# Kernel tuning notes

Measured on AMD Instinct MI355X. Metric: run time of the kernel, lower is better.

Reference implementation:

```python
import jax, jax.numpy as jnp
import numpy as np

N = 30000      # nodes
E = 480000     # edges (before self-loops)
D = 100        # hidden_dim / in_channels
H = 4          # heads
PH = 100       # per-head dim
L = 6          # layers
G = 128        # graphs in batch
NUM_ATOM = 100
OUT_DIM = 64


def _xavier(k, shape, gain=1.0):
    fan_in, fan_out = shape[-1], shape[-2]
    lim = gain * np.sqrt(6.0 / (fan_in + fan_out))
    return jax.random.uniform(k, shape, jnp.float32, -lim, lim)


def setup_inputs() -> dict:
    key = jax.random.key(0)
    ks = jax.random.split(key, 12)
    x = jax.random.randint(ks[0], (N,), 0, NUM_ATOM)
    edge_index = jax.random.randint(ks[1], (2, E), 0, N)
    edge_attr = jax.random.normal(ks[2], (E, D), dtype=jnp.float32)
    batch = jnp.sort(jax.random.randint(ks[3], (N,), 0, G))
    emb = _xavier(ks[4], (NUM_ATOM, D))
    W = _xavier(ks[5], (L, H * PH, D))
    We = _xavier(ks[6], (L, H * PH, D))
    a = _xavier(ks[7], (L, H, 2 * PH), gain=1.414)
    ln_g = jnp.ones((L, D), jnp.float32)
    ln_b = jnp.zeros((L, D), jnp.float32)
    w1 = _xavier(ks[8], (OUT_DIM, D))
    b1 = jnp.zeros((OUT_DIM,), jnp.float32)
    w2 = _xavier(ks[9], (1, OUT_DIM))
    b2 = jnp.zeros((1,), jnp.float32)
    return dict(x=x, edge_index=edge_index, edge_attr=edge_attr, batch=batch,
                emb=emb, W=W, We=We, a=a, ln_g=ln_g, ln_b=ln_b,
                w1=w1, b1=b1, w2=w2, b2=b2)


def _forward(x, edge_index, edge_attr, batch, emb, W, We, a, ln_g, ln_b, w1, b1, w2, b2):
    n = x.shape[0]
    loop = jnp.arange(n)
    src = jnp.concatenate([edge_index[0], loop])            # [E']
    dst = jnp.concatenate([edge_index[1], loop])            # [E']  (target, softmax key)
    ea = jnp.concatenate([edge_attr, jnp.zeros((n, D), edge_attr.dtype)], axis=0)  # self-loop attr = 0
    h = emb[x]                                              # [N, D]
    for l in range(L):
        hx = (h @ W[l].T).reshape(n, H, PH)                 # [N, H, PH]
        he = (ea @ We[l].T).reshape(-1, H, PH)              # [E', H, PH]
        a_i, a_j = a[l][:, :PH], a[l][:, PH:]               # [H, PH] each
        # alpha = sum(a * [x_i ; x_j + edge_attr]) split into two dots
        score_i = jnp.einsum('nhd,hd->nh', hx, a_i)         # [N, H]
        xj = hx[src]                                        # [E', H, PH]
        alpha = score_i[dst] + jnp.einsum('ehd,hd->eh', xj + he, a_j)  # [E', H]
        alpha = jnp.where(alpha > 0, alpha, 0.2 * alpha)    # leaky_relu(0.2)
        # segment softmax over edges grouped by target node (every node has a self-loop)
        amax = jax.ops.segment_max(alpha, dst, num_segments=n)
        alpha = jnp.exp(alpha - amax[dst])
        denom = jax.ops.segment_sum(alpha, dst, num_segments=n)
        alpha = alpha / (denom[dst] + 1e-16)
        msg = (xj * alpha[..., None]).sum(axis=1)           # [E', PH] (heads summed, per module)
        aggr = jax.ops.segment_sum(msg, dst, num_segments=n)  # [N, PH]
        # LayerNorm(D), eps=1e-5
        mu = aggr.mean(-1, keepdims=True)
        var = ((aggr - mu) ** 2).mean(-1, keepdims=True)
        y = (aggr - mu) / jnp.sqrt(var + 1e-5) * ln_g[l] + ln_b[l]
        y = jax.nn.elu(y)                                   # dropout = identity (eval)
        h = y + h
    # global mean pool over graphs
    s = jax.ops.segment_sum(h, batch, num_segments=G)
    cnt = jax.ops.segment_sum(jnp.ones((n, 1), h.dtype), batch, num_segments=G)
    pooled = s / jnp.maximum(cnt, 1.0)
    hh = pooled @ w1.T + b1                                 # [G, 64]
    out = hh @ w2.T + b2                                    # [G, 1]
    return out, hh


def reference(x, edge_index, edge_attr, batch, emb, W, We, a, ln_g, ln_b, w1, b1, w2, b2):
    return _forward(x, edge_index, edge_attr, batch, emb, W, We, a, ln_g, ln_b, w1, b1, w2, b2)
```

## Files before the change

kernel.cpp:

```cpp
#include <hip/hip_runtime.h>
#include <cstdint>
#include <cstddef>

#define N_NODES 30000
#define N_EDGES 480000
#define EP_EDGES (N_EDGES + N_NODES)
#define DIM 100
#define NH 4
#define NL 6
#define NG 128
#define KP 416

#define OFF_H       0u
#define OFF_AGG2    12000000u
#define OFF_POS     12000000u
#define OFF_DEG     13920000u
#define OFF_CURS    14040000u
#define OFF_POOL    12000000u
#define OFF_CNT     12051200u
#define OFF_SCI     60000000u
#define OFF_SCJ     60480000u
#define OFF_ESC     60960000u
#define OFF_CWIJ    85440000u
#define OFF_CWE     85459200u
#define OFF_WR      85469184u
#define OFF_INDPTR  86429184u
#define OFF_CSRS    86549248u
#define OFF_BSUM    88589248u

typedef _Float16 half8 __attribute__((ext_vector_type(8)));
typedef float f32x4 __attribute__((ext_vector_type(4)));

static __device__ __forceinline__ unsigned short f2h(float f) {
  return __builtin_bit_cast(unsigned short, (_Float16)f);
}
static __device__ __forceinline__ float h2f(unsigned short u) {
  return (float)__builtin_bit_cast(_Float16, u);
}

__global__ __launch_bounds__(256) void k_init(const int* __restrict__ x,
                                              const float* __restrict__ emb,
                                              float* __restrict__ h,
                                              int* __restrict__ deg, int* __restrict__ cursor) {
  int tid = blockIdx.x * 256 + threadIdx.x;
  if (tid < N_NODES * DIM) {
    int n = tid / DIM;
    int d = tid - n * DIM;
    h[tid] = emb[x[n] * DIM + d];
  }
  if (tid < N_NODES) { deg[tid] = 0; cursor[tid] = 0; }
}

__global__ __launch_bounds__(256) void k_fold(const float* __restrict__ W,
                                              const float* __restrict__ We,
                                              const float* __restrict__ a,
                                              float* __restrict__ cWij, float* __restrict__ cWe) {
  int tid = blockIdx.x * 256 + threadIdx.x;
  if (tid < NL * DIM * 8) {
    int l = tid / 800, r = tid % 800;
    int k = r >> 3, c = r & 7;
    int hh = c & 3, isJ = c >> 2;
    const float* wp = W + (size_t)(l * 400 + hh * 100) * 100 + k;
    const float* ap = a + (size_t)(l * 4 + hh) * 200 + isJ * 100;
    float s = 0.f;
    for (int d = 0; d < 100; ++d) s += wp[(size_t)d * 100] * ap[d];
    cWij[l * 800 + k * 8 + c] = s;
  } else if (tid < NL * DIM * 8 + DIM * 24) {
    int m = tid - NL * DIM * 8;
    int k = m / 24, c = m % 24;
    int l = c >> 2, hh = c & 3;
    const float* wp = We + (size_t)(l * 400 + hh * 100) * 100 + k;
    const float* ap = a + (size_t)(l * 4 + hh) * 200 + 100;
    float s = 0.f;
    for (int d = 0; d < 100; ++d) s += wp[(size_t)d * 100] * ap[d];
    cWe[c * 104 + k] = s;
  }
}

__global__ __launch_bounds__(256) void k_bfrag(const float* __restrict__ W,
                                               unsigned short* __restrict__ Bfrag) {
  int tid = blockIdx.x * 256 + threadIdx.x;
  if (tid >= NL * 7 * 13 * 64 * 8) return;
  int j = tid & 7;
  int lane = (tid >> 3) & 63;
  int rest = tid >> 9;
  int ks = rest % 13;
  int rest2 = rest / 13;
  int ct = rest2 % 7;
  int l = rest2 / 7;
  int k = ks * 32 + ((lane >> 4) << 3) + j;
  int n = ct * 16 + (lane & 15);
  float v = 0.f;
  if (k < 400 && n < 100) {
    int hh = k / 100, kk = k - hh * 100;
    v = W[(size_t)(l * 400 + hh * 100 + n) * 100 + kk];
  }
  Bfrag[tid] = f2h(v);
}

__global__ __launch_bounds__(256) void k_deg(const int* __restrict__ ei, int* __restrict__ deg) {
  int tid = blockIdx.x * 256 + threadIdx.x;
  if (tid >= EP_EDGES) return;
  int dstn = (tid < N_EDGES) ? ei[N_EDGES + tid] : (tid - N_EDGES);
  atomicAdd(&deg[dstn], 1);
}

__global__ __launch_bounds__(1024) void k_scan1(const int* __restrict__ deg,
                                                int* __restrict__ indptr, int* __restrict__ bsum) {
  __shared__ int s[1024];
  int t = threadIdx.x;
  int i = blockIdx.x * 1024 + t;
  int v = (i < N_NODES) ? deg[i] : 0;
  s[t] = v;
  __syncthreads();
  for (int off = 1; off < 1024; off <<= 1) {
    int tmp = (t >= off) ? s[t - off] : 0;
    __syncthreads();
    s[t] += tmp;
    __syncthreads();
  }
  if (i < N_NODES) indptr[i + 1] = s[t];
  if (t == 1023) bsum[blockIdx.x] = s[1023];
}
__global__ __launch_bounds__(64) void k_scan2(int* __restrict__ bsum) {
  int t = threadIdx.x;
  int v = (t < 30) ? bsum[t] : 0;
  int inc = v;
  for (int off = 1; off < 64; off <<= 1) {
    int up = __shfl_up(inc, off);
    if (t >= off) inc += up;
  }
  if (t < 30) bsum[t] = inc - v;
}
__global__ __launch_bounds__(1024) void k_scan3(int* __restrict__ indptr,
                                                const int* __restrict__ bsum) {
  int i = blockIdx.x * 1024 + threadIdx.x;
  if (i < N_NODES) indptr[i + 1] += bsum[blockIdx.x];
  if (i == 0) indptr[0] = 0;
}

__global__ __launch_bounds__(256) void k_scatter(const int* __restrict__ ei,
                                                 const int* __restrict__ indptr,
                                                 int* __restrict__ cursor,
                                                 int* __restrict__ csr_src,
                                                 int* __restrict__ pos,
                                                 unsigned short* __restrict__ esc) {
  int tid = blockIdx.x * 256 + threadIdx.x;
  if (tid >= EP_EDGES) return;
  int dstn = (tid < N_EDGES) ? ei[N_EDGES + tid] : (tid - N_EDGES);
  int srcn = (tid < N_EDGES) ? ei[tid] : (tid - N_EDGES);
  int p = indptr[dstn] + atomicAdd(&cursor[dstn], 1);
  csr_src[p] = srcn;
  if (tid < N_EDGES) {
    pos[tid] = p;
  } else {
#pragma unroll
    for (int l = 0; l < NL; ++l) {
      ushort4 z; z.x = 0; z.y = 0; z.z = 0; z.w = 0;
      *(ushort4*)(esc + ((size_t)l * EP_EDGES + p) * 4) = z;
    }
  }
}

__global__ __launch_bounds__(384) void k_escore(const float* __restrict__ ea,
                                                const float* __restrict__ cWe,
                                                const int* __restrict__ pos,
                                                unsigned short* __restrict__ esc) {
  __shared__ __align__(16) float s_ea[64 * 100];
  int t = threadIdx.x;
  const float4* g4 = (const float4*)(ea + (size_t)blockIdx.x * 6400);
  float4* l4 = (float4*)s_ea;
  for (int i = t; i < 1600; i += 384) l4[i] = g4[i];
  __syncthreads();

  int slot = t & 63;
  int lg = __builtin_amdgcn_readfirstlane(t >> 6);
  const float* r0 = s_ea + slot * 100;
  const float* wl = cWe + (lg * 4) * 104;
  float acc0[4] = {0.f, 0.f, 0.f, 0.f};
#pragma unroll
  for (int k4 = 0; k4 < 25; ++k4) {
    float4 x0 = *(const float4*)(r0 + k4 * 4);
#pragma unroll
    for (int hh = 0; hh < 4; ++hh) {
      float4 w = *(const float4*)(wl + hh * 104 + k4 * 4);
      acc0[hh] = fmaf(x0.w, w.w, fmaf(x0.z, w.z, fmaf(x0.y, w.y, fmaf(x0.x, w.x, acc0[hh]))));
    }
  }
  int e0 = blockIdx.x * 64 + slot;
  int p0 = pos[e0];
  ushort4 o0;
  o0.x = f2h(acc0[0]); o0.y = f2h(acc0[1]); o0.z = f2h(acc0[2]); o0.w = f2h(acc0[3]);
  *(ushort4*)(esc + ((size_t)lg * EP_EDGES + p0) * 4) = o0;
}

__global__ __launch_bounds__(256) void k_score(const float* __restrict__ h,
                                               const float* __restrict__ cw,
                                               float* __restrict__ sc_i, float* __restrict__ sc_j) {
  __shared__ __align__(16) float s[DIM * 8];
  for (int i = threadIdx.x; i < DIM * 8; i += 256) s[i] = cw[i];
  __syncthreads();
  int n = blockIdx.x * 256 + threadIdx.x;
  if (n >= N_NODES) return;
  float acc[8] = {0.f, 0.f, 0.f, 0.f, 0.f, 0.f, 0.f, 0.f};
  const float* hr = h + (size_t)n * DIM;
  for (int k4 = 0; k4 < 25; ++k4) {
    float4 v = *(const float4*)(hr + k4 * 4);
    float vv[4] = {v.x, v.y, v.z, v.w};
#pragma unroll
    for (int kk = 0; kk < 4; ++kk) {
      const float* sr = s + (k4 * 4 + kk) * 8;
#pragma unroll
      for (int c = 0; c < 8; ++c) acc[c] += vv[kk] * sr[c];
    }
  }
  *(float4*)(sc_i + (size_t)n * 4) = make_float4(acc[0], acc[1], acc[2], acc[3]);
  *(float4*)(sc_j + (size_t)n * 4) = make_float4(acc[4], acc[5], acc[6], acc[7]);
}

#define ALPHA_P(pp)                                                                  \
  int s_ = csr_src[pp];                                                              \
  float4 sj_ = *(const float4*)(sc_j + (size_t)s_ * 4);                              \
  ushort4 eb_ = *(const ushort4*)(esc_l + (size_t)(pp) * 4);                         \
  float a0 = si.x + sj_.x + h2f(eb_.x); a0 = a0 > 0.f ? a0 : 0.2f * a0;              \
  float a1 = si.y + sj_.y + h2f(eb_.y); a1 = a1 > 0.f ? a1 : 0.2f * a1;              \
  float a2 = si.z + sj_.z + h2f(eb_.z); a2 = a2 > 0.f ? a2 : 0.2f * a2;              \
  float a3 = si.w + sj_.w + h2f(eb_.w); a3 = a3 > 0.f ? a3 : 0.2f * a3;

__global__ __launch_bounds__(256) void k_aggr(const float* __restrict__ h,
                                              const float* __restrict__ sc_i,
                                              const float* __restrict__ sc_j,
                                              const unsigned short* __restrict__ esc_l,
                                              const int* __restrict__ indptr,
                                              const int* __restrict__ csr_src,
                                              unsigned short* __restrict__ agg2h) {
  __shared__ __align__(16) uint4 s_pack[4][64];
  int wave = threadIdx.x >> 6;
  int lane = threadIdx.x & 63;
  int n = blockIdx.x * 4 + wave;
  int start = indptr[n], end = indptr[n + 1];
  int deg = end - start;
  float4 si = *(const float4*)(sc_i + (size_t)n * 4);
  float A0 = 0.f, A1 = 0.f, A2 = 0.f, A3 = 0.f;
  float B0 = 0.f, B1 = 0.f, B2 = 0.f, B3 = 0.f;
  bool has2 = lane < (DIM - 64);

  if (deg <= 64) {
    int p = start + lane;
    bool act = p < end;
    int srcr = 0;
    float a0 = -1e30f, a1 = -1e30f, a2 = -1e30f, a3 = -1e30f;
    if (act) {
      int s2 = csr_src[p];
      float4 sj2 = *(const float4*)(sc_j + (size_t)s2 * 4);
      ushort4 eb2 = *(const ushort4*)(esc_l + (size_t)p * 4);
      a0 = si.x + sj2.x + h2f(eb2.x); a0 = a0 > 0.f ? a0 : 0.2f * a0;
      a1 = si.y + sj2.y + h2f(eb2.y); a1 = a1 > 0.f ? a1 : 0.2f * a1;
      a2 = si.z + sj2.z + h2f(eb2.z); a2 = a2 > 0.f ? a2 : 0.2f * a2;
      a3 = si.w + sj2.w + h2f(eb2.w); a3 = a3 > 0.f ? a3 : 0.2f * a3;
      srcr = s2;
    }
    float m0 = a0, m1 = a1, m2 = a2, m3 = a3;
    for (int off = 32; off; off >>= 1) {
      m0 = fmaxf(m0, __shfl_xor(m0, off));
      m1 = fmaxf(m1, __shfl_xor(m1, off));
      m2 = fmaxf(m2, __shfl_xor(m2, off));
      m3 = fmaxf(m3, __shfl_xor(m3, off));
    }
    float e0 = act ? __expf(a0 - m0) : 0.f;
    float e1 = act ? __expf(a1 - m1) : 0.f;
    float e2 = act ? __expf(a2 - m2) : 0.f;
    float e3 = act ? __expf(a3 - m3) : 0.f;
    float d0 = e0, d1 = e1, d2 = e2, d3 = e3;
    for (int off = 32; off; off >>= 1) {
      d0 += __shfl_xor(d0, off); d1 += __shfl_xor(d1, off);
      d2 += __shfl_xor(d2, off); d3 += __shfl_xor(d3, off);
    }
    float w0 = e0 * (1.f / (d0 + 1e-16f));
    float w1 = e1 * (1.f / (d1 + 1e-16f));
    float w2 = e2 * (1.f / (d2 + 1e-16f));
    float w3 = e3 * (1.f / (d3 + 1e-16f));
    uint4 pk;
    pk.x = (unsigned)srcr;
    pk.y = (unsigned)f2h(w0) | ((unsigned)f2h(w1) << 16);
    pk.z = (unsigned)f2h(w2) | ((unsigned)f2h(w3) << 16);
    pk.w = 0u;
    s_pack[wave][lane] = pk;
    for (int j = 0; j < deg; ++j) {
      uint4 pk2 = s_pack[wave][j];
      int sj2 = (int)pk2.x;
      float q0 = h2f((unsigned short)(pk2.y & 0xffffu));
      float q1 = h2f((unsigned short)(pk2.y >> 16));
      float q2 = h2f((unsigned short)(pk2.z & 0xffffu));
      float q3 = h2f((unsigned short)(pk2.z >> 16));
      const float* hr = h + (size_t)sj2 * DIM;
      float hv0 = hr[lane];
      float hv1 = has2 ? hr[64 + lane] : 0.f;
      A0 += q0 * hv0; A1 += q1 * hv0; A2 += q2 * hv0; A3 += q3 * hv0;
      B0 += q0 * hv1; B1 += q1 * hv1; B2 += q2 * hv1; B3 += q3 * hv1;
    }
  } else {
    float m0 = -1e30f, m1 = -1e30f, m2 = -1e30f, m3 = -1e30f;
    for (int p = start + lane; p < end; p += 64) {
      ALPHA_P(p)
      (void)s_;
      m0 = fmaxf(m0, a0); m1 = fmaxf(m1, a1); m2 = fmaxf(m2, a2); m3 = fmaxf(m3, a3);
    }
    for (int off = 32; off; off >>= 1) {
      m0 = fmaxf(m0, __shfl_xor(m0, off));
      m1 = fmaxf(m1, __shfl_xor(m1, off));
      m2 = fmaxf(m2, __shfl_xor(m2, off));
      m3 = fmaxf(m3, __shfl_xor(m3, off));
    }
    float d0 = 0.f, d1 = 0.f, d2 = 0.f, d3 = 0.f;
    for (int p = start + lane; p < end; p += 64) {
      ALPHA_P(p)
      (void)s_;
      d0 += __expf(a0 - m0); d1 += __expf(a1 - m1);
      d2 += __expf(a2 - m2); d3 += __expf(a3 - m3);
    }
    for (int off = 32; off; off >>= 1) {
      d0 += __shfl_xor(d0, off); d1 += __shfl_xor(d1, off);
      d2 += __shfl_xor(d2, off); d3 += __shfl_xor(d3, off);
    }
    float i0 = 1.f / (d0 + 1e-16f), i1 = 1.f / (d1 + 1e-16f);
    float i2 = 1.f / (d2 + 1e-16f), i3 = 1.f / (d3 + 1e-16f);
    for (int base = start; base < end; base += 64) {
      int cntv = min(64, end - base);
      int p = base + lane;
      float w0 = 0.f, w1 = 0.f, w2 = 0.f, w3 = 0.f;
      int srcr = 0;
      if (p < end) {
        ALPHA_P(p)
        w0 = __expf(a0 - m0) * i0; w1 = __expf(a1 - m1) * i1;
        w2 = __expf(a2 - m2) * i2; w3 = __expf(a3 - m3) * i3;
        srcr = s_;
      }
      for (int j = 0; j < cntv; ++j) {
        int sj2 = __shfl(srcr, j);
        float q0 = __shfl(w0, j), q1 = __shfl(w1, j);
        float q2 = __shfl(w2, j), q3 = __shfl(w3, j);
        const float* hr = h + (size_t)sj2 * DIM;
        float hv0 = hr[lane];
        float hv1 = has2 ? hr[64 + lane] : 0.f;
        A0 += q0 * hv0; A1 += q1 * hv0; A2 += q2 * hv0; A3 += q3 * hv0;
        B0 += q0 * hv1; B1 += q1 * hv1; B2 += q2 * hv1; B3 += q3 * hv1;
      }
    }
  }
  unsigned short* outp = agg2h + (size_t)n * KP;
  outp[lane] = f2h(A0); outp[100 + lane] = f2h(A1);
  outp[200 + lane] = f2h(A2); outp[300 + lane] = f2h(A3);
  if (has2) {
    outp[64 + lane] = f2h(B0); outp[164 + lane] = f2h(B1);
    outp[264 + lane] = f2h(B2); outp[364 + lane] = f2h(B3);
  }
  if (lane < KP - 400) outp[400 + lane] = 0;
}

__global__ __launch_bounds__(256) void k_gemm2(const _Float16* __restrict__ agg2h,
                                               const _Float16* __restrict__ Bfrag_l,
                                               const float* __restrict__ lg,
                                               const float* __restrict__ lb,
                                               float* __restrict__ h) {
  int t = threadIdx.x;
  int lane = t & 63;
  int w = t >> 6;
  int c = lane & 15;
  int quad = lane >> 4;
  int nb = blockIdx.x * 64 + w * 16;

  f32x4 acc[7];
#pragma unroll
  for (int ct = 0; ct < 7; ++ct) acc[ct] = (f32x4){0.f, 0.f, 0.f, 0.f};

  const _Float16* arow = agg2h + (size_t)(nb + c) * KP + quad * 8;
#pragma unroll
  for (int ks = 0; ks < 13; ++ks) {
    half8 a = *(const half8*)(arow + ks * 32);
    const _Float16* bp = Bfrag_l + (size_t)(ks * 64 + lane) * 8;
#pragma unroll
    for (int ct = 0; ct < 7; ++ct) {
      half8 b = *(const half8*)(bp + (size_t)ct * 13 * 64 * 8);
      acc[ct] = __builtin_amdgcn_mfma_f32_16x16x32_f16(a, b, acc[ct], 0, 0, 0);
    }
  }

  float gv[7], bv[7];
#pragma unroll
  for (int ct = 0; ct < 7; ++ct) {
    int col = ct * 16 + c;
    gv[ct] = (col < DIM) ? lg[col] : 0.f;
    bv[ct] = (col < DIM) ? lb[col] : 0.f;
  }
  bool c4 = c < 4;
#pragma unroll
  for (int r = 0; r < 4; ++r) {
    int n = nb + quad * 4 + r;
    float v[7];
#pragma unroll
    for (int ct = 0; ct < 7; ++ct) v[ct] = acc[ct][r];
    float s = v[0] + v[1] + v[2] + v[3] + v[4] + v[5] + (c4 ? v[6] : 0.f);
    s += __shfl_xor(s, 1); s += __shfl_xor(s, 2);
    s += __shfl_xor(s, 4); s += __shfl_xor(s, 8);
    float mu = s * 0.01f;
    float dv[7];
    float s2 = 0.f;
#pragma unroll
    for (int ct = 0; ct < 6; ++ct) { dv[ct] = v[ct] - mu; s2 += dv[ct] * dv[ct]; }
    dv[6] = c4 ? (v[6] - mu) : 0.f;
    s2 += dv[6] * dv[6];
    s2 += __shfl_xor(s2, 1); s2 += __shfl_xor(s2, 2);
    s2 += __shfl_xor(s2, 4); s2 += __shfl_xor(s2, 8);
    float rstd = rsqrtf(s2 * 0.01f + 1e-5f);
    if (n < N_NODES) {
      float* hp = h + (size_t)n * DIM;
#pragma unroll
      for (int ct = 0; ct < 7; ++ct) {
        int col = ct * 16 + c;
        if (ct < 6 || c4) {
          float y = dv[ct] * rstd * gv[ct] + bv[ct];
          y = y > 0.f ? y : (__expf(y) - 1.f);
          hp[col] += y;
        }
      }
    }
  }
}

__global__ __launch_bounds__(128) void k_pool(const float* __restrict__ h,
                                              const int* __restrict__ batch,
                                              float* __restrict__ pooled, float* __restrict__ cnt) {
  int d = threadIdx.x;
  int n0 = blockIdx.x * 64;
  int n1 = min(n0 + 64, N_NODES);
  if (n0 >= N_NODES) return;
  int curg = -1;
  float acc = 0.f, c = 0.f;
  for (int n = n0; n < n1; ++n) {
    int g = batch[n];
    if (g != curg) {
      if (curg >= 0) {
        if (d < 100) atomicAdd(&pooled[(size_t)curg * DIM + d], acc);
        if (d == 0) atomicAdd(&cnt[curg], c);
      }
      curg = g; acc = 0.f; c = 0.f;
    }
    if (d < 100) acc += h[(size_t)n * DIM + d];
    c += 1.f;
  }
  if (curg >= 0) {
    if (d < 100) atomicAdd(&pooled[(size_t)curg * DIM + d], acc);
    if (d == 0) atomicAdd(&cnt[curg], c);
  }
}

__global__ __launch_bounds__(64) void k_mlp(const float* __restrict__ pooled,
                                            const float* __restrict__ cnt,
                                            const float* __restrict__ w1, const float* __restrict__ b1,
                                            const float* __restrict__ w2, const float* __restrict__ b2,
                                            float* __restrict__ out) {
  int g = blockIdx.x;
  int j = threadIdx.x;
  float invc = 1.0f / fmaxf(cnt[g], 1.0f);
  const float* pr = pooled + (size_t)g * DIM;
  const float* wr = w1 + (size_t)j * DIM;
  float acc = 0.f;
  for (int k = 0; k < DIM; ++k) acc += pr[k] * wr[k];
  float hh = acc * invc + b1[j];
  out[NG + g * 64 + j] = hh;
  float v = hh * w2[j];
  for (int off = 32; off; off >>= 1) v += __shfl_xor(v, off);
  if (j == 0) out[g] = v + b2[0];
}

extern "C" void kernel_launch(void* const* d_in, const int* in_sizes, int n_in,
                              void* d_out, int out_size, void* d_ws, size_t ws_size,
                              hipStream_t stream) {
  (void)in_sizes; (void)n_in; (void)out_size; (void)ws_size;
  const int* x = (const int*)d_in[0];
  const int* ei = (const int*)d_in[1];
  const float* ea = (const float*)d_in[2];
  const int* batch = (const int*)d_in[3];
  const float* emb = (const float*)d_in[4];
  const float* W = (const float*)d_in[5];
  const float* We = (const float*)d_in[6];
  const float* a = (const float*)d_in[7];
  const float* ln_g = (const float*)d_in[8];
  const float* ln_b = (const float*)d_in[9];
  const float* w1 = (const float*)d_in[10];
  const float* b1 = (const float*)d_in[11];
  const float* w2 = (const float*)d_in[12];
  const float* b2 = (const float*)d_in[13];
  float* outp = (float*)d_out;

  char* ws = (char*)d_ws;
  float* h = (float*)(ws + OFF_H);
  unsigned short* agg2h = (unsigned short*)(ws + OFF_AGG2);
  int* pos = (int*)(ws + OFF_POS);
  int* deg = (int*)(ws + OFF_DEG);
  int* cursor = (int*)(ws + OFF_CURS);
  float* pooled = (float*)(ws + OFF_POOL);
  float* cnt = (float*)(ws + OFF_CNT);
  float* sc_i = (float*)(ws + OFF_SCI);
  float* sc_j = (float*)(ws + OFF_SCJ);
  unsigned short* esc = (unsigned short*)(ws + OFF_ESC);
  float* cWij = (float*)(ws + OFF_CWIJ);
  float* cWe = (float*)(ws + OFF_CWE);
  unsigned short* Bfrag = (unsigned short*)(ws + OFF_WR);
  int* indptr = (int*)(ws + OFF_INDPTR);
  int* csr_src = (int*)(ws + OFF_CSRS);
  int* bsum = (int*)(ws + OFF_BSUM);

  k_init<<<11719, 256, 0, stream>>>(x, emb, h, deg, cursor);
  k_fold<<<29, 256, 0, stream>>>(W, We, a, cWij, cWe);
  k_bfrag<<<1092, 256, 0, stream>>>(W, Bfrag);
  k_deg<<<1993, 256, 0, stream>>>(ei, deg);
  k_scan1<<<30, 1024, 0, stream>>>(deg, indptr, bsum);
  k_scan2<<<1, 64, 0, stream>>>(bsum);
  k_scan3<<<30, 1024, 0, stream>>>(indptr, bsum);
  k_scatter<<<1993, 256, 0, stream>>>(ei, indptr, cursor, csr_src, pos, esc);
  k_escore<<<7500, 384, 0, stream>>>(ea, cWe, pos, esc);

  for (int l = 0; l < NL; ++l) {
    k_score<<<118, 256, 0, stream>>>(h, cWij + l * 800, sc_i, sc_j);
    k_aggr<<<7500, 256, 0, stream>>>(h, sc_i, sc_j, esc + (size_t)l * EP_EDGES * 4,
                                     indptr, csr_src, agg2h);
    k_gemm2<<<469, 256, 0, stream>>>((const _Float16*)agg2h,
                                     (const _Float16*)(Bfrag + (size_t)l * 7 * 13 * 64 * 8),
                                     ln_g + l * 100, ln_b + l * 100, h);
  }

  hipMemsetAsync(ws + OFF_POOL, 0, 51200 + 512, stream);
  k_pool<<<469, 128, 0, stream>>>(h, batch, pooled, cnt);
  k_mlp<<<128, 64, 0, stream>>>(pooled, cnt, w1, b1, w2, b2, outp);
}
```

Baseline: 851.2 us.

## Compute edge scores in CSR order via gathered edge ids, writing all layers coalesced

The scatter kernel now records the original edge id for each CSR slot instead of a position per edge. Edge scores are computed per CSR slot by gathering that edge's attribute row, with one thread producing all 24 layer-head scores. This makes the fp16 score writes coalesced and replaces the separate zero-fill of self-loop slots. In exchange, reads of the 192 MB edge-attribute array become per-thread strided gathers in random order rather than tile loads through shared memory.

```diff
diff --git a/kernel.cpp b/kernel.cpp
--- a/kernel.cpp
+++ b/kernel.cpp
@@ -13,9 +13,9 @@
 
 #define OFF_H       0u
 #define OFF_AGG2    12000000u
-#define OFF_POS     12000000u
-#define OFF_DEG     13920000u
-#define OFF_CURS    14040000u
+#define OFF_EID     12000000u
+#define OFF_DEG     14040000u
+#define OFF_CURS    14160000u
 #define OFF_POOL    12000000u
 #define OFF_CNT     12051200u
 #define OFF_SCI     60000000u
@@ -54,7 +54,7 @@
 __global__ __launch_bounds__(256) void k_fold(const float* __restrict__ W,
                                               const float* __restrict__ We,
                                               const float* __restrict__ a,
-                                              float* __restrict__ cWij, float* __restrict__ cWe) {
+                                              float* __restrict__ cWij, float* __restrict__ cWe2) {
   int tid = blockIdx.x * 256 + threadIdx.x;
   if (tid < NL * DIM * 8) {
     int l = tid / 800, r = tid % 800;
@@ -73,7 +73,7 @@
     const float* ap = a + (size_t)(l * 4 + hh) * 200 + 100;
     float s = 0.f;
     for (int d = 0; d < 100; ++d) s += wp[(size_t)d * 100] * ap[d];
-    cWe[c * 104 + k] = s;
+    cWe2[((k >> 2) * 24 + c) * 4 + (k & 3)] = s;
   }
 }
 
@@ -143,55 +143,46 @@
                                                  const int* __restrict__ indptr,
                                                  int* __restrict__ cursor,
                                                  int* __restrict__ csr_src,
-                                                 int* __restrict__ pos,
-                                                 unsigned short* __restrict__ esc) {
+                                                 int* __restrict__ csr_eid) {
   int tid = blockIdx.x * 256 + threadIdx.x;
   if (tid >= EP_EDGES) return;
   int dstn = (tid < N_EDGES) ? ei[N_EDGES + tid] : (tid - N_EDGES);
   int srcn = (tid < N_EDGES) ? ei[tid] : (tid - N_EDGES);
   int p = indptr[dstn] + atomicAdd(&cursor[dstn], 1);
   csr_src[p] = srcn;
-  if (tid < N_EDGES) {
-    pos[tid] = p;
-  } else {
+  csr_eid[p] = (tid < N_EDGES) ? tid : -1;
+}
+
+__global__ __launch_bounds__(256) void k_escore(const float* __restrict__ ea,
+                                                const float* __restrict__ cWe2,
+                                                const int* __restrict__ csr_eid,
+                                                unsigned short* __restrict__ esc) {
+  int slot = blockIdx.x * 256 + threadIdx.x;
+  int e = (slot < EP_EDGES) ? csr_eid[slot] : -1;
+  float acc[24];
+#pragma unroll
+  for (int c = 0; c < 24; ++c) acc[c] = 0.f;
+  if (e >= 0) {
+    const float4* rp = (const float4*)(ea + (size_t)e * DIM);
+    for (int k4 = 0; k4 < 25; ++k4) {
+      float4 x = rp[k4];
+      const float4* wp = (const float4*)(cWe2 + k4 * 96);
+#pragma unroll
+      for (int c = 0; c < 24; ++c) {
+        float4 w = wp[c];
+        acc[c] = fmaf(x.w, w.w, fmaf(x.z, w.z, fmaf(x.y, w.y, fmaf(x.x, w.x, acc[c]))));
+      }
+    }
+  }
+  if (slot < EP_EDGES) {
 #pragma unroll
     for (int l = 0; l < NL; ++l) {
-      ushort4 z; z.x = 0; z.y = 0; z.z = 0; z.w = 0;
-      *(ushort4*)(esc + ((size_t)l * EP_EDGES + p) * 4) = z;
-    }
-  }
-}
-
-__global__ __launch_bounds__(384) void k_escore(const float* __restrict__ ea,
-                                                const float* __restrict__ cWe,
-                                                const int* __restrict__ pos,
-                                                unsigned short* __restrict__ esc) {
-  __shared__ __align__(16) float s_ea[64 * 100];
-  int t = threadIdx.x;
-  const float4* g4 = (const float4*)(ea + (size_t)blockIdx.x * 6400);
-  float4* l4 = (float4*)s_ea;
-  for (int i = t; i < 1600; i += 384) l4[i] = g4[i];
-  __syncthreads();
-
-  int slot = t & 63;
-  int lg = __builtin_amdgcn_readfirstlane(t >> 6);
-  const float* r0 = s_ea + slot * 100;
-  const float* wl = cWe + (lg * 4) * 104;
-  float acc0[4] = {0.f, 0.f, 0.f, 0.f};
-#pragma unroll
-  for (int k4 = 0; k4 < 25; ++k4) {
-    float4 x0 = *(const float4*)(r0 + k4 * 4);
-#pragma unroll
-    for (int hh = 0; hh < 4; ++hh) {
-      float4 w = *(const float4*)(wl + hh * 104 + k4 * 4);
-      acc0[hh] = fmaf(x0.w, w.w, fmaf(x0.z, w.z, fmaf(x0.y, w.y, fmaf(x0.x, w.x, acc0[hh]))));
-    }
-  }
-  int e0 = blockIdx.x * 64 + slot;
-  int p0 = pos[e0];
-  ushort4 o0;
-  o0.x = f2h(acc0[0]); o0.y = f2h(acc0[1]); o0.z = f2h(acc0[2]); o0.w = f2h(acc0[3]);
-  *(ushort4*)(esc + ((size_t)lg * EP_EDGES + p0) * 4) = o0;
+      ushort4 o;
+      o.x = f2h(acc[l * 4 + 0]); o.y = f2h(acc[l * 4 + 1]);
+      o.z = f2h(acc[l * 4 + 2]); o.w = f2h(acc[l * 4 + 3]);
+      *(ushort4*)(esc + ((size_t)l * EP_EDGES + slot) * 4) = o;
+    }
+  }
 }
 
 __global__ __launch_bounds__(256) void k_score(const float* __restrict__ h,
@@ -497,7 +488,7 @@
   char* ws = (char*)d_ws;
   float* h = (float*)(ws + OFF_H);
   unsigned short* agg2h = (unsigned short*)(ws + OFF_AGG2);
-  int* pos = (int*)(ws + OFF_POS);
+  int* csr_eid = (int*)(ws + OFF_EID);
   int* deg = (int*)(ws + OFF_DEG);
   int* cursor = (int*)(ws + OFF_CURS);
   float* pooled = (float*)(ws + OFF_POOL);
@@ -506,21 +497,21 @@
   float* sc_j = (float*)(ws + OFF_SCJ);
   unsigned short* esc = (unsigned short*)(ws + OFF_ESC);
   float* cWij = (float*)(ws + OFF_CWIJ);
-  float* cWe = (float*)(ws + OFF_CWE);
+  float* cWe2 = (float*)(ws + OFF_CWE);
   unsigned short* Bfrag = (unsigned short*)(ws + OFF_WR);
   int* indptr = (int*)(ws + OFF_INDPTR);
   int* csr_src = (int*)(ws + OFF_CSRS);
   int* bsum = (int*)(ws + OFF_BSUM);
 
   k_init<<<11719, 256, 0, stream>>>(x, emb, h, deg, cursor);
-  k_fold<<<29, 256, 0, stream>>>(W, We, a, cWij, cWe);
+  k_fold<<<29, 256, 0, stream>>>(W, We, a, cWij, cWe2);
   k_bfrag<<<1092, 256, 0, stream>>>(W, Bfrag);
   k_deg<<<1993, 256, 0, stream>>>(ei, deg);
   k_scan1<<<30, 1024, 0, stream>>>(deg, indptr, bsum);
   k_scan2<<<1, 64, 0, stream>>>(bsum);
   k_scan3<<<30, 1024, 0, stream>>>(indptr, bsum);
-  k_scatter<<<1993, 256, 0, stream>>>(ei, indptr, cursor, csr_src, pos, esc);
-  k_escore<<<7500, 384, 0, stream>>>(ea, cWe, pos, esc);
+  k_scatter<<<1993, 256, 0, stream>>>(ei, indptr, cursor, csr_src, csr_eid);
+  k_escore<<<1993, 256, 0, stream>>>(ea, cWe2, csr_eid, esc);
 
   for (int l = 0; l < NL; ++l) {
     k_score<<<118, 256, 0, stream>>>(h, cWij + l * 800, sc_i, sc_j);
```

Measured after the change: 955.9 us. +12.3%, slower.
